# Optimization experiments

Hardware: AMD Instinct MI355X
Metric: run time of the kernel (lower is better)

The kernel has to match this reference:

```python
import jax, jax.numpy as jnp
import numpy as np

RAW_ID_SPACE = 500_000   # raw id universe (fill_max)
MAX_VOCAB = 1_000_000    # max_vocabulary_size (rows of embedding_var)
EMB_DIM = 128            # embedding_vec_size
IDS_SHAPE = (4096, 26, 8)


def setup_inputs() -> dict:
    key = jax.random.key(0)
    k1, k2 = jax.random.split(key)
    ids = jax.random.randint(k1, IDS_SHAPE, 0, RAW_ID_SPACE, dtype=jnp.int32)
    embedding_var = jax.random.uniform(
        k2, (MAX_VOCAB, EMB_DIM), dtype=jnp.float32, minval=-0.05, maxval=0.05)
    default_embedding = jnp.zeros((1, EMB_DIM), dtype=jnp.float32)
    return {"ids": ids, "embedding_var": embedding_var,
            "default_embedding": default_embedding}


def reference(ids, embedding_var, default_embedding):
    # Training path of HashtableEmbedding.call starting from an empty hash
    # table and counter=0: each raw id is assigned a slot equal to its
    # first-appearance rank in the flattened id stream (tf.unique order),
    # then embeddings are gathered at those slots.
    flat = ids.reshape(-1)                       # [N]
    n = flat.shape[0]
    pos = jnp.arange(n, dtype=jnp.int32)
    # first occurrence position of each raw id (scatter-min over raw space)
    first_pos = jax.ops.segment_min(pos, flat, num_segments=RAW_ID_SPACE)
    fp = first_pos[flat]                         # [N] first pos of my id
    is_first = (fp == pos)
    rank = jnp.cumsum(is_first.astype(jnp.int32)) - 1  # first-appearance rank
    hash_ids = rank[fp]                          # [N] slot in [0, n_unique)
    # table = [embedding_var ; default_embedding]; slot V selects default row
    table = jnp.concatenate([embedding_var, default_embedding], axis=0)
    emb = table[hash_ids]                        # [N, D] irregular gather
    return emb.reshape(ids.shape + (embedding_var.shape[1],))
```

## Files before the change

### kernel.cpp

```cpp
#include <hip/hip_runtime.h>

#define N_IDS   851968
#define RAW     500000
#define EMB_DIM 128
#define EPB     1024
#define NBLK    (N_IDS / EPB)

__device__ __forceinline__ int wave_incl_scan(int v) {
    int lane = threadIdx.x & 63;
#pragma unroll
    for (int d = 1; d < 64; d <<= 1) {
        int n = __shfl_up(v, d, 64);
        if (lane >= d) v += n;
    }
    return v;
}

__global__ void k_first_pos(const int* __restrict__ flat, int* __restrict__ first_pos) {
    int i = blockIdx.x * 256 + threadIdx.x;
    if (i < N_IDS) atomicMin(&first_pos[flat[i]], i);
}

__global__ void k_block_sums(const int* __restrict__ flat, const int* __restrict__ first_pos,
                             int* __restrict__ bsums) {
    int tid = threadIdx.x;
    int4 f4 = reinterpret_cast<const int4*>(flat)[blockIdx.x * 256 + tid];
    int base = blockIdx.x * EPB + tid * 4;
    int s = 0;
    s += (first_pos[f4.x] == base + 0);
    s += (first_pos[f4.y] == base + 1);
    s += (first_pos[f4.z] == base + 2);
    s += (first_pos[f4.w] == base + 3);
#pragma unroll
    for (int d = 32; d >= 1; d >>= 1) s += __shfl_down(s, d, 64);
    __shared__ int wsum[4];
    int wid = tid >> 6, lane = tid & 63;
    if (lane == 0) wsum[wid] = s;
    __syncthreads();
    if (tid == 0) bsums[blockIdx.x] = wsum[0] + wsum[1] + wsum[2] + wsum[3];
}

__global__ void k_scan_sums(const int* __restrict__ bsums, int* __restrict__ boff) {
    int tid = threadIdx.x;
    int v = (tid < NBLK) ? bsums[tid] : 0;
    int incl = wave_incl_scan(v);
    __shared__ int wsum[16];
    int wid = tid >> 6, lane = tid & 63;
    if (lane == 63) wsum[wid] = incl;
    __syncthreads();
    int woff = 0;
    for (int w = 0; w < wid; ++w) woff += wsum[w];
    if (tid < NBLK) boff[tid] = woff + incl - v;
}

__global__ void k_rank_slot(const int* __restrict__ flat, const int* __restrict__ first_pos,
                            const int* __restrict__ boff, int* __restrict__ slot) {
    int tid = threadIdx.x;
    int4 f4 = reinterpret_cast<const int4*>(flat)[blockIdx.x * 256 + tid];
    int base = blockIdx.x * EPB + tid * 4;
    int f[4] = {f4.x, f4.y, f4.z, f4.w};
    int flg[4], s = 0;
#pragma unroll
    for (int j = 0; j < 4; ++j) {
        flg[j] = (first_pos[f[j]] == base + j);
        s += flg[j];
    }
    int incl = wave_incl_scan(s);
    __shared__ int wsum[4];
    int wid = tid >> 6, lane = tid & 63;
    if (lane == 63) wsum[wid] = incl;
    __syncthreads();
    int woff = 0;
    for (int w = 0; w < wid; ++w) woff += wsum[w];
    int off = boff[blockIdx.x] + woff + (incl - s);
#pragma unroll
    for (int j = 0; j < 4; ++j) {
        if (flg[j]) { slot[f[j]] = off; ++off; }
    }
}

__global__ void k_gather(const int* __restrict__ flat, const int* __restrict__ slot,
                         const float4* __restrict__ emb, float4* __restrict__ out) {
    int t = blockIdx.x * 256 + threadIdx.x;
    int row = t >> 5;
    int c = t & 31;
    int s = slot[flat[row]];
    out[t] = emb[(size_t)s * 32 + c];
}

extern "C" void kernel_launch(void* const* d_in, const int* in_sizes, int n_in,
                              void* d_out, int out_size, void* d_ws, size_t ws_size,
                              hipStream_t stream) {
    const int*   ids = (const int*)d_in[0];
    const float* emb = (const float*)d_in[1];

    char* ws = (char*)d_ws;
    int* first_pos = (int*)(ws);
    int* slot      = (int*)(ws + 2000000);
    int* bsums     = (int*)(ws + 4000000);
    int* boff      = (int*)(ws + 4003328);

    hipMemsetAsync(first_pos, 0x7F, (size_t)RAW * sizeof(int), stream);

    k_first_pos <<<(N_IDS + 255) / 256, 256, 0, stream>>>(ids, first_pos);
    k_block_sums<<<NBLK, 256, 0, stream>>>(ids, first_pos, bsums);
    k_scan_sums <<<1, 1024, 0, stream>>>(bsums, boff);
    k_rank_slot <<<NBLK, 256, 0, stream>>>(ids, first_pos, boff, slot);
    k_gather    <<<(N_IDS * 32) / 256, 256, 0, stream>>>(ids, slot,
                     (const float4*)emb, (float4*)d_out);
}
```

Measured before the change: 233.0 us.

## Precompute per-row slots and gather four rows per thread with nontemporal stores

Adds a kernel that resolves each id's slot once into a per-row array, so the gather no longer does a double indirection per float4. The gather kernel now handles four float4 elements per thread, strided by a quarter of the output, to keep more independent loads in flight. Output writes use nontemporal stores so they do not pollute the cache. This costs an extra kernel launch plus a small intermediate buffer round trip through memory.

Result: faster. 194.3 us (-16.6%).

```diff
diff --git a/kernel.cpp b/kernel.cpp
--- a/kernel.cpp
+++ b/kernel.cpp
@@ -5,6 +5,9 @@
 #define EMB_DIM 128
 #define EPB     1024
 #define NBLK    (N_IDS / EPB)
+#define TOTAL_F4 (N_IDS * 32)
+
+typedef float f32x4 __attribute__((ext_vector_type(4)));
 
 __device__ __forceinline__ int wave_incl_scan(int v) {
     int lane = threadIdx.x & 63;
@@ -79,13 +82,29 @@
     }
 }
 
-__global__ void k_gather(const int* __restrict__ flat, const int* __restrict__ slot,
-                         const float4* __restrict__ emb, float4* __restrict__ out) {
+__global__ void k_row_slot(const int* __restrict__ flat, const int* __restrict__ slot,
+                           int* __restrict__ rslot) {
+    int i = blockIdx.x * 256 + threadIdx.x;
+    rslot[i] = slot[flat[i]];
+}
+
+__global__ void k_gather(const int* __restrict__ rslot,
+                         const f32x4* __restrict__ emb, f32x4* __restrict__ out) {
+    const int stride = TOTAL_F4 / 4;
     int t = blockIdx.x * 256 + threadIdx.x;
-    int row = t >> 5;
-    int c = t & 31;
-    int s = slot[flat[row]];
-    out[t] = emb[(size_t)s * 32 + c];
+    int i0 = t, i1 = t + stride, i2 = t + 2 * stride, i3 = t + 3 * stride;
+    int r0 = rslot[i0 >> 5];
+    int r1 = rslot[i1 >> 5];
+    int r2 = rslot[i2 >> 5];
+    int r3 = rslot[i3 >> 5];
+    f32x4 v0 = emb[(size_t)r0 * 32 + (i0 & 31)];
+    f32x4 v1 = emb[(size_t)r1 * 32 + (i1 & 31)];
+    f32x4 v2 = emb[(size_t)r2 * 32 + (i2 & 31)];
+    f32x4 v3 = emb[(size_t)r3 * 32 + (i3 & 31)];
+    __builtin_nontemporal_store(v0, &out[i0]);
+    __builtin_nontemporal_store(v1, &out[i1]);
+    __builtin_nontemporal_store(v2, &out[i2]);
+    __builtin_nontemporal_store(v3, &out[i3]);
 }
 
 extern "C" void kernel_launch(void* const* d_in, const int* in_sizes, int n_in,
@@ -99,13 +118,15 @@
     int* slot      = (int*)(ws + 2000000);
     int* bsums     = (int*)(ws + 4000000);
     int* boff      = (int*)(ws + 4003328);
+    int* rslot     = (int*)(ws + 4006656);
 
-    hipMemsetAsync(first_pos, 0x7F, (size_t)RAW * sizeof(int), stream);
+    (void)hipMemsetAsync(first_pos, 0x7F, (size_t)RAW * sizeof(int), stream);
 
     k_first_pos <<<(N_IDS + 255) / 256, 256, 0, stream>>>(ids, first_pos);
     k_block_sums<<<NBLK, 256, 0, stream>>>(ids, first_pos, bsums);
     k_scan_sums <<<1, 1024, 0, stream>>>(bsums, boff);
     k_rank_slot <<<NBLK, 256, 0, stream>>>(ids, first_pos, boff, slot);
-    k_gather    <<<(N_IDS * 32) / 256, 256, 0, stream>>>(ids, slot,
-                     (const float4*)emb, (float4*)d_out);
+    k_row_slot  <<<N_IDS / 256, 256, 0, stream>>>(ids, slot, rslot);
+    k_gather    <<<(TOTAL_F4 / 4) / 256, 256, 0, stream>>>(rslot,
+                     (const f32x4*)emb, (f32x4*)d_out);
 }
```
